# Optimization experiments

Hardware: AMD Instinct MI355X
Metric: run time of the kernel (lower is better)

## Reference

```python
import jax, jax.numpy as jnp
from jax import lax
import numpy as np

B, HW = 256, 64          # batch, image side (grayscale)
L, E, K = 32, 64, 8192   # latent_size, embedding_size, num_embeddings
DN = ('NHWC', 'HWIO', 'NHWC')


def setup_inputs() -> dict:
    key = jax.random.key(0)
    ks = jax.random.split(key, 21)
    n = lambda k, shape, s=0.05: (jax.random.normal(k, shape, jnp.float32) * s)
    return {
        'x': jax.random.uniform(ks[0], (B, HW, HW), jnp.float32),
        # encoder convs (SAME, stride 2): 64->32->16->8
        'enc_w1': n(ks[1], (4, 4, 1, 32)),   'enc_b1': jnp.zeros((32,), jnp.float32),
        'enc_w2': n(ks[2], (4, 4, 32, 64)),  'enc_b2': jnp.zeros((64,), jnp.float32),
        'enc_w3': n(ks[3], (4, 4, 64, 128)), 'enc_b3': jnp.zeros((128,), jnp.float32),
        # encoder dense: flatten 8*8*128=8192 -> 512 -> L*E=2048
        'fc_w': n(ks[4], (8192, 512), 0.02), 'fc_b': jnp.zeros((512,), jnp.float32),
        'ffc_w': n(ks[5], (512, L * E), 0.02), 'ffc_b': jnp.zeros((L * E,), jnp.float32),
        # VQ codebook
        'embeds': n(ks[6], (K, E), 0.02),
        # decoder dense: 2048 -> 512, then 1x1x512 feature map
        'dec_fc_w': n(ks[7], (L * E, 512), 0.02), 'dec_fc_b': jnp.zeros((512,), jnp.float32),
        # decoder conv_transpose VALID: 1->4->16->64
        'dec_w1': n(ks[8], (4, 4, 512, 256)),  'dec_b1': jnp.zeros((256,), jnp.float32),
        'dec_w2': n(ks[9], (4, 4, 256, 128)),  'dec_b2': jnp.zeros((128,), jnp.float32),
        'dec_w3': n(ks[10], (4, 4, 128, 1)),   'dec_b3': jnp.zeros((1,), jnp.float32),
    }


def _conv(h, w, b, s):
    return jax.nn.relu(lax.conv_general_dilated(h, w, (s, s), 'SAME', dimension_numbers=DN) + b)


def reference(x, enc_w1, enc_b1, enc_w2, enc_b2, enc_w3, enc_b3,
              fc_w, fc_b, ffc_w, ffc_b, embeds,
              dec_fc_w, dec_fc_b, dec_w1, dec_b1, dec_w2, dec_b2, dec_w3, dec_b3):
    # ---- encoder ----
    h = x[..., None]                                   # (B,64,64,1)
    h = _conv(h, enc_w1, enc_b1, 2)                    # (B,32,32,32)
    h = _conv(h, enc_w2, enc_b2, 2)                    # (B,16,16,64)
    h = _conv(h, enc_w3, enc_b3, 2)                    # (B,8,8,128)
    h = h.reshape(h.shape[0], -1)                      # (B,8192)
    h = jax.nn.relu(h @ fc_w + fc_b)                   # (B,512)
    pred = jax.nn.relu(h @ ffc_w + ffc_b).reshape(-1, L, E)  # (B,L,E)
    # ---- VQ middle: nearest codebook entry (argmin of L2 norm == argmin of squared dist) ----
    d2 = (jnp.sum(pred * pred, axis=-1, keepdims=True)
          - 2.0 * jnp.einsum('ble,ke->blk', pred, embeds)
          + jnp.sum(embeds * embeds, axis=-1))         # (B,L,K)
    classes = jnp.argmin(d2, axis=-1)                  # (B,L) int
    collected = embeds[classes]                        # (B,L,E) gather
    h = collected.reshape(-1, L * E)                   # (B,2048)
    # ---- decoder ----
    h = jax.nn.relu(h @ dec_fc_w + dec_fc_b)           # (B,512)
    h = h[:, None, None, :]                            # (B,1,1,512)
    h = jax.nn.relu(lax.conv_transpose(h, dec_w1, (1, 1), 'VALID', dimension_numbers=DN) + dec_b1)  # (B,4,4,256)
    h = jax.nn.relu(lax.conv_transpose(h, dec_w2, (4, 4), 'VALID', dimension_numbers=DN) + dec_b2)  # (B,16,16,128)
    out = lax.conv_transpose(h, dec_w3, (4, 4), 'VALID', dimension_numbers=DN) + dec_b3             # (B,64,64,1)
    return out  # L2 loss_type: output_t = logits_t
```

## Files before the change

kernel.cpp:

```cpp
#include <hip/hip_runtime.h>
#include <cfloat>


typedef short bf16x8 __attribute__((ext_vector_type(8)));
typedef float f32x4 __attribute__((ext_vector_type(4)));
#define MFMA16(a, b, c) __builtin_amdgcn_mfma_f32_16x16x32_bf16(a, b, c, 0, 0, 0)

__device__ inline unsigned short f2bf(float x) {
  unsigned u = __float_as_uint(x);
  u += 0x7fffu + ((u >> 16) & 1u);
  return (unsigned short)(u >> 16);
}
__device__ inline float bf2f(unsigned short h) {
  return __uint_as_float(((unsigned)h) << 16);
}
__device__ inline void split3v(float v, unsigned short& hb, unsigned short& mb,
                               unsigned short& lb) {
  hb = f2bf(v);
  float r1 = v - bf2f(hb);
  mb = f2bf(r1);
  lb = f2bf(r1 - bf2f(mb));
}

__global__ __launch_bounds__(256) void k_zborder(unsigned short* __restrict__ base,
                                                 int W, size_t planeElems,
                                                 int logC) {
  int bc = blockIdx.x * 256 + threadIdx.x;
  int C = 1 << logC;
  int b = bc >> logC, c = bc & (C - 1);
  int i = blockIdx.y, row, col;
  if (i < W) { row = 0; col = i; }
  else if (i < 2 * W) { row = W - 1; col = i - W; }
  else { int j = i - 2 * W; row = 1 + (j >> 1); col = (j & 1) ? W - 1 : 0; }
  base[blockIdx.z * planeElems + ((size_t)(b * W + row) * W + col) * C + c] = 0;
}

__global__ __launch_bounds__(256) void k_conv1(const float* __restrict__ x,
                                               const float* __restrict__ w,
                                               const float* __restrict__ bias,
                                               unsigned short* __restrict__ oH,
                                               unsigned short* __restrict__ oM,
                                               unsigned short* __restrict__ oL) {
  int b = blockIdx.x >> 5;
  int y = blockIdx.x & 31;
  int t = threadIdx.x;
  int c = t & 31;
  int xg = t >> 5;
  float acc[4] = {0.f, 0.f, 0.f, 0.f};
  for (int dy = 0; dy < 4; ++dy) {
    int iy = 2 * y + dy - 1;
    if (iy < 0 || iy >= 64) continue;
    const float* xrow = x + ((size_t)b * 64 + iy) * 64;
    for (int dx = 0; dx < 4; ++dx) {
      float wv = w[(dy * 4 + dx) * 32 + c];
#pragma unroll
      for (int i = 0; i < 4; ++i) {
        int ix = 8 * xg + 2 * i + dx - 1;
        float v = (ix >= 0 && ix < 64) ? xrow[ix] : 0.f;
        acc[i] = fmaf(v, wv, acc[i]);
      }
    }
  }
  float bv = bias[c];
#pragma unroll
  for (int i = 0; i < 4; ++i) {
    float v = acc[i] + bv;
    v = v > 0.f ? v : 0.f;
    unsigned short hb, mb, lb;
    split3v(v, hb, mb, lb);
    size_t o = ((size_t)(b * 34 + y + 1) * 34 + (4 * xg + i + 1)) * 32 + c;
    oH[o] = hb; oM[o] = mb; oL[o] = lb;
  }
}

__global__ __launch_bounds__(256) void k_wprep2(const float* __restrict__ w,
                                                unsigned short* __restrict__ H,
                                                unsigned short* __restrict__ M,
                                                unsigned short* __restrict__ L) {
  int idx = blockIdx.x * 256 + threadIdx.x;
  int j = idx & 7, lane = (idx >> 3) & 63, nt = (idx >> 9) & 3, s = idx >> 11;
  int ci = ((lane >> 4) << 3) + j, co = (nt << 4) + (lane & 15);
  unsigned short hb, mb, lb;
  split3v(w[(s * 32 + ci) * 64 + co], hb, mb, lb);
  H[idx] = hb; M[idx] = mb; L[idx] = lb;
}
__global__ __launch_bounds__(256) void k_wprep3(const float* __restrict__ w,
                                                unsigned short* __restrict__ H,
                                                unsigned short* __restrict__ M,
                                                unsigned short* __restrict__ L) {
  int idx = blockIdx.x * 256 + threadIdx.x;
  int j = idx & 7, lane = (idx >> 3) & 63, ks = (idx >> 9) & 1;
  int nt = (idx >> 10) & 3, ch = (idx >> 12) & 1, s = idx >> 13;
  int ci = ks * 32 + ((lane >> 4) << 3) + j;
  int co = ch * 64 + (nt << 4) + (lane & 15);
  unsigned short hb, mb, lb;
  split3v(w[(s * 64 + ci) * 128 + co], hb, mb, lb);
  H[idx] = hb; M[idx] = mb; L[idx] = lb;
}

__global__ __launch_bounds__(256) void k_conv2m(
    const unsigned short* __restrict__ aH, const unsigned short* __restrict__ aM,
    const unsigned short* __restrict__ aL, const unsigned short* __restrict__ wH,
    const unsigned short* __restrict__ wM, const unsigned short* __restrict__ wL,
    const float* __restrict__ bias, unsigned short* __restrict__ oH,
    unsigned short* __restrict__ oM, unsigned short* __restrict__ oL) {
  int t = threadIdx.x;
  int wave = t >> 6, lane = t & 63;
  int l15 = lane & 15, quad = lane >> 4;
  int m0 = blockIdx.x * 64 + wave * 16;
  int p = m0 + l15;
  int b = p >> 8, y = (p >> 4) & 15, x = p & 15;
  f32x4 acc[4] = {};
  for (int s = 0; s < 16; ++s) {
    int dy = s >> 2, dx = s & 3;
    size_t aoff = ((size_t)(b * 34 + 2 * y + dy) * 34 + (2 * x + dx)) * 32 + quad * 8;
    bf16x8 ah = *(const bf16x8*)(aH + aoff);
    bf16x8 am = *(const bf16x8*)(aM + aoff);
    bf16x8 al = *(const bf16x8*)(aL + aoff);
#pragma unroll
    for (int nt = 0; nt < 4; ++nt) {
      size_t woff = ((size_t)(s * 4 + nt) * 64 + lane) * 8;
      bf16x8 bh = *(const bf16x8*)(wH + woff);
      bf16x8 bm = *(const bf16x8*)(wM + woff);
      bf16x8 bl = *(const bf16x8*)(wL + woff);
      acc[nt] = MFMA16(am, bm, acc[nt]);
      acc[nt] = MFMA16(ah, bl, acc[nt]);
      acc[nt] = MFMA16(al, bh, acc[nt]);
      acc[nt] = MFMA16(ah, bm, acc[nt]);
      acc[nt] = MFMA16(am, bh, acc[nt]);
      acc[nt] = MFMA16(ah, bh, acc[nt]);
    }
  }
#pragma unroll
  for (int r = 0; r < 4; ++r) {
    int pp = m0 + quad * 4 + r;
    int b2 = pp >> 8, yo = (pp >> 4) & 15, xo = pp & 15;
    size_t obase = ((size_t)(b2 * 18 + yo + 1) * 18 + (xo + 1)) * 64;
#pragma unroll
    for (int nt = 0; nt < 4; ++nt) {
      int co = nt * 16 + l15;
      float v = acc[nt][r] + bias[co];
      v = v > 0.f ? v : 0.f;
      unsigned short hb, mb, lb;
      split3v(v, hb, mb, lb);
      oH[obase + co] = hb; oM[obase + co] = mb; oL[obase + co] = lb;
    }
  }
}

__global__ __launch_bounds__(256) void k_conv3m(
    const unsigned short* __restrict__ aH, const unsigned short* __restrict__ aM,
    const unsigned short* __restrict__ aL, const unsigned short* __restrict__ wH,
    const unsigned short* __restrict__ wM, const unsigned short* __restrict__ wL,
    const float* __restrict__ bias, unsigned short* __restrict__ oH,
    unsigned short* __restrict__ oM, unsigned short* __restrict__ oL) {
  int t = threadIdx.x;
  int wave = t >> 6, lane = t & 63;
  int l15 = lane & 15, quad = lane >> 4;
  int pg = wave >> 1, ch = wave & 1;
  int m0 = blockIdx.x * 64 + pg * 32;
  f32x4 acc[2][4] = {};
  for (int s = 0; s < 16; ++s) {
    int dy = s >> 2, dx = s & 3;
    bf16x8 ah[2][2], am[2][2], al[2][2];
#pragma unroll
    for (int mt = 0; mt < 2; ++mt) {
      int p = m0 + mt * 16 + l15;
      int b = p >> 6, y = (p >> 3) & 7, x = p & 7;
      size_t base = ((size_t)(b * 18 + 2 * y + dy) * 18 + (2 * x + dx)) * 64 + quad * 8;
#pragma unroll
      for (int ks = 0; ks < 2; ++ks) {
        ah[mt][ks] = *(const bf16x8*)(aH + base + ks * 32);
        am[mt][ks] = *(const bf16x8*)(aM + base + ks * 32);
        al[mt][ks] = *(const bf16x8*)(aL + base + ks * 32);
      }
    }
#pragma unroll
    for (int nt = 0; nt < 4; ++nt) {
#pragma unroll
      for (int ks = 0; ks < 2; ++ks) {
        size_t woff = ((size_t)((((s * 2 + ch) * 4 + nt) * 2 + ks) * 64 + lane)) * 8;
        bf16x8 bh = *(const bf16x8*)(wH + woff);
        bf16x8 bm = *(const bf16x8*)(wM + woff);
        bf16x8 bl = *(const bf16x8*)(wL + woff);
#pragma unroll
        for (int mt = 0; mt < 2; ++mt) {
          acc[mt][nt] = MFMA16(am[mt][ks], bm, acc[mt][nt]);
          acc[mt][nt] = MFMA16(ah[mt][ks], bl, acc[mt][nt]);
          acc[mt][nt] = MFMA16(al[mt][ks], bh, acc[mt][nt]);
          acc[mt][nt] = MFMA16(ah[mt][ks], bm, acc[mt][nt]);
          acc[mt][nt] = MFMA16(am[mt][ks], bh, acc[mt][nt]);
          acc[mt][nt] = MFMA16(ah[mt][ks], bh, acc[mt][nt]);
        }
      }
    }
  }
#pragma unroll
  for (int mt = 0; mt < 2; ++mt)
#pragma unroll
    for (int nt = 0; nt < 4; ++nt) {
      int co = ch * 64 + nt * 16 + l15;
      float bv = bias[co];
#pragma unroll
      for (int r = 0; r < 4; ++r) {
        int pp = m0 + mt * 16 + quad * 4 + r;
        float v = acc[mt][nt][r] + bv;
        v = v > 0.f ? v : 0.f;
        unsigned short hb, mb, lb;
        split3v(v, hb, mb, lb);
        size_t o = (size_t)pp * 128 + co;
        oH[o] = hb; oM[o] = mb; oL[o] = lb;
      }
    }
}

__global__ __launch_bounds__(256) void k_bprep(const float* __restrict__ w,
                                               unsigned short* __restrict__ Bp,
                                               int K, int N, int NP) {
  int idx = blockIdx.x * 256 + threadIdx.x;
  if (idx >= NP * K * N) return;
  int j = idx & 7, lane = (idx >> 3) & 63;
  int f = idx >> 9;
  int NT = N >> 4, KT = K >> 5;
  int ntg = f % NT; f /= NT;
  int kt = f % KT; int s = f / KT;
  int k = kt * 32 + ((lane >> 4) << 3) + j;
  int n = ntg * 16 + (lane & 15);
  unsigned short hb, mb, lb;
  split3v(w[(size_t)k * N + n], hb, mb, lb);
  Bp[idx] = s == 0 ? hb : (s == 1 ? mb : lb);
}

__global__ __launch_bounds__(256) void k_bprep_ct(const float* __restrict__ w,
                                                  unsigned short* __restrict__ Bp,
                                                  int K, int N, int oshift,
                                                  int NP) {
  int idx = blockIdx.x * 256 + threadIdx.x;
  if (idx >= NP * K * N) return;
  int j = idx & 7, lane = (idx >> 3) & 63;
  int f = idx >> 9;
  int NT = N >> 4, KT = K >> 5;
  int ntg = f % NT; f /= NT;
  int kt = f % KT; int s = f / KT;
  int k = kt * 32 + ((lane >> 4) << 3) + j;
  int n = ntg * 16 + (lane & 15);
  int o = n & ((1 << oshift) - 1), ru = n >> oshift;
  int r = ru >> 2, u = ru & 3;
  int sf = (3 - r) * 4 + (3 - u);
  unsigned short hb, mb, lb;
  split3v(w[(((size_t)sf * K + k) << oshift) + o], hb, mb, lb);
  Bp[idx] = s == 0 ? hb : (s == 1 ? mb : lb);
}

template <int NP, int NTW>
__global__ __launch_bounds__(256) void k_mgemm(
    const unsigned short* __restrict__ A0, const unsigned short* __restrict__ A1,
    const unsigned short* __restrict__ A2, const unsigned short* __restrict__ Bp,
    float* __restrict__ C, const float* __restrict__ bias,
    int M, int N, int K, int bmask) {
  int S = gridDim.z;
  int Kc = K / S;
  int t = threadIdx.x;
  int wave = t >> 6, lane = t & 63;
  int l15 = lane & 15, quad = lane >> 4;
  int m0 = blockIdx.x * 64 + wave * 16;
  int n0 = blockIdx.y * (16 * NTW);
  int KT = K >> 5, NT = N >> 4;
  int kt0 = (blockIdx.z * Kc) >> 5;
  int ktn = Kc >> 5;
  size_t sstride = (size_t)KT * NT * 512;
  const unsigned short* arow0 = A0 + (size_t)(m0 + l15) * K + quad * 8;
  const unsigned short* arow1 = A1 + (size_t)(m0 + l15) * K + quad * 8;
  const unsigned short* arow2 = nullptr;
  if constexpr (NP == 3) arow2 = A2 + (size_t)(m0 + l15) * K + quad * 8;
  f32x4 acc[NTW] = {};
  for (int kt = kt0; kt < kt0 + ktn; ++kt) {
    bf16x8 ah = *(const bf16x8*)(arow0 + kt * 32);
    bf16x8 am = *(const bf16x8*)(arow1 + kt * 32);
    bf16x8 al;
    if constexpr (NP == 3) al = *(const bf16x8*)(arow2 + kt * 32);
    const unsigned short* bbase =
        Bp + ((size_t)kt * NT + (n0 >> 4)) * 512 + lane * 8;
#pragma unroll
    for (int nt = 0; nt < NTW; ++nt) {
      const unsigned short* bp = bbase + nt * 512;
      bf16x8 bh = *(const bf16x8*)(bp);
      bf16x8 bm = *(const bf16x8*)(bp + sstride);
      if constexpr (NP == 3) {
        bf16x8 bl = *(const bf16x8*)(bp + 2 * sstride);
        acc[nt] = MFMA16(am, bm, acc[nt]);
        acc[nt] = MFMA16(ah, bl, acc[nt]);
        acc[nt] = MFMA16(al, bh, acc[nt]);
        acc[nt] = MFMA16(ah, bm, acc[nt]);
        acc[nt] = MFMA16(am, bh, acc[nt]);
        acc[nt] = MFMA16(ah, bh, acc[nt]);
      } else {
        acc[nt] = MFMA16(ah, bm, acc[nt]);
        acc[nt] = MFMA16(am, bh, acc[nt]);
        acc[nt] = MFMA16(ah, bh, acc[nt]);
      }
    }
  }
  if (S == 1) {
#pragma unroll
    for (int nt = 0; nt < NTW; ++nt) {
      int n = n0 + nt * 16 + l15;
      float bv = bias[n & bmask];
#pragma unroll
      for (int r = 0; r < 4; ++r) {
        int m = m0 + quad * 4 + r;
        float v = acc[nt][r] + bv;
        C[(size_t)m * N + n] = v > 0.f ? v : 0.f;
      }
    }
  } else {
    float* Cp = C + (size_t)blockIdx.z * M * N;
#pragma unroll
    for (int nt = 0; nt < NTW; ++nt) {
      int n = n0 + nt * 16 + l15;
#pragma unroll
      for (int r = 0; r < 4; ++r) {
        int m = m0 + quad * 4 + r;
        Cp[(size_t)m * N + n] = acc[nt][r];
      }
    }
  }
}

template <int NPOUT>
__global__ __launch_bounds__(256) void k_sumrelu3(
    const float* __restrict__ part, const float* __restrict__ bias,
    unsigned short* __restrict__ oH, unsigned short* __restrict__ oM,
    unsigned short* __restrict__ oL, int MN, int bmask, int S) {
  int idx = blockIdx.x * 256 + threadIdx.x;
  float s = 0.f;
  for (int z = 0; z < S; ++z) s += part[(size_t)z * MN + idx];
  s += bias[idx & bmask];
  s = s > 0.f ? s : 0.f;
  unsigned short hb = f2bf(s);
  float r1 = s - bf2f(hb);
  unsigned short mb = f2bf(r1);
  oH[idx] = hb; oM[idx] = mb;
  if constexpr (NPOUT == 3) oL[idx] = f2bf(r1 - bf2f(mb));
}

__global__ __launch_bounds__(256) void k_norm2(const float* __restrict__ e,
                                               float* __restrict__ n2) {
  int k = blockIdx.x * 256 + threadIdx.x;
  const float4* p = (const float4*)(e + (size_t)k * 64);
  float s0 = 0, s1 = 0, s2 = 0, s3 = 0;
#pragma unroll
  for (int j = 0; j < 16; ++j) {
    float4 v = p[j];
    s0 = fmaf(v.x, v.x, s0); s1 = fmaf(v.y, v.y, s1);
    s2 = fmaf(v.z, v.z, s2); s3 = fmaf(v.w, v.w, s3);
  }
  n2[k] = (s0 + s1) + (s2 + s3);
}

__global__ __launch_bounds__(256) void k_eprep(const float* __restrict__ e,
                                               unsigned short* __restrict__ Bp) {
  int idx = blockIdx.x * 256 + threadIdx.x;
  int j = idx & 7, lane = (idx >> 3) & 63;
  int f = idx >> 9;
  int s = f % 3; f /= 3;
  int nt = f % 4; f /= 4;
  int ks = f % 2; int kt = f / 2;
  int code = kt * 64 + nt * 16 + (lane & 15);
  int k = ks * 32 + ((lane >> 4) << 3) + j;
  unsigned short hb, mb, lb;
  split3v(e[(size_t)code * 64 + k], hb, mb, lb);
  Bp[idx] = s == 0 ? hb : (s == 1 ? mb : lb);
}

__global__ __launch_bounds__(256) void k_vqmfma3(
    const unsigned short* __restrict__ pH, const unsigned short* __restrict__ pM,
    const unsigned short* __restrict__ pL, const unsigned short* __restrict__ eB,
    const float* __restrict__ n2, float* __restrict__ pbd, int* __restrict__ pbk) {
  int t = threadIdx.x;
  int wave = t >> 6, lane = t & 63;
  int l15 = lane & 15, quad = lane >> 4;
  int m0 = blockIdx.x * 128 + wave * 32;
  int z = blockIdx.y;
  bf16x8 ah[2][2], am[2][2], al[2][2];
#pragma unroll
  for (int mt = 0; mt < 2; ++mt) {
    size_t arow = (size_t)(m0 + mt * 16 + l15) * 64 + quad * 8;
#pragma unroll
    for (int ks = 0; ks < 2; ++ks) {
      ah[mt][ks] = *(const bf16x8*)(pH + arow + ks * 32);
      am[mt][ks] = *(const bf16x8*)(pM + arow + ks * 32);
      al[mt][ks] = *(const bf16x8*)(pL + arow + ks * 32);
    }
  }
  float bd[2][4]; int bk[2][4];
#pragma unroll
  for (int mt = 0; mt < 2; ++mt)
#pragma unroll
    for (int r = 0; r < 4; ++r) { bd[mt][r] = FLT_MAX; bk[mt][r] = 0; }
  for (int kt = z * 16; kt < z * 16 + 16; ++kt) {
    const unsigned short* bb = eB + (size_t)kt * 12288 + lane * 8;
    f32x4 acc[2][4] = {};
#pragma unroll
    for (int ks = 0; ks < 2; ++ks)
#pragma unroll
      for (int nt = 0; nt < 4; ++nt) {
        const unsigned short* bp = bb + ((ks * 4 + nt) * 3) * 512;
        bf16x8 bh = *(const bf16x8*)(bp);
        bf16x8 bm = *(const bf16x8*)(bp + 512);
        bf16x8 bl = *(const bf16x8*)(bp + 1024);
#pragma unroll
        for (int mt = 0; mt < 2; ++mt) {
          acc[mt][nt] = MFMA16(am[mt][ks], bm, acc[mt][nt]);
          acc[mt][nt] = MFMA16(ah[mt][ks], bl, acc[mt][nt]);
          acc[mt][nt] = MFMA16(al[mt][ks], bh, acc[mt][nt]);
          acc[mt][nt] = MFMA16(ah[mt][ks], bm, acc[mt][nt]);
          acc[mt][nt] = MFMA16(am[mt][ks], bh, acc[mt][nt]);
          acc[mt][nt] = MFMA16(ah[mt][ks], bh, acc[mt][nt]);
        }
      }
    int cb = kt * 64;
#pragma unroll
    for (int nt = 0; nt < 4; ++nt) {
      int code = cb + nt * 16 + l15;
      float nv = n2[code];
#pragma unroll
      for (int mt = 0; mt < 2; ++mt)
#pragma unroll
        for (int r = 0; r < 4; ++r) {
          float d = fmaf(-2.f, acc[mt][nt][r], nv);
          if (d < bd[mt][r]) { bd[mt][r] = d; bk[mt][r] = code; }
        }
    }
  }
#pragma unroll
  for (int mt = 0; mt < 2; ++mt)
#pragma unroll
    for (int r = 0; r < 4; ++r)
#pragma unroll
      for (int s = 1; s < 16; s <<= 1) {
        float od = __shfl_xor(bd[mt][r], s);
        int ok = __shfl_xor(bk[mt][r], s);
        if (od < bd[mt][r] || (od == bd[mt][r] && ok < bk[mt][r])) {
          bd[mt][r] = od; bk[mt][r] = ok;
        }
      }
  if (l15 == 0) {
#pragma unroll
    for (int mt = 0; mt < 2; ++mt)
#pragma unroll
      for (int r = 0; r < 4; ++r) {
        pbd[(size_t)z * 8192 + m0 + mt * 16 + quad * 4 + r] = bd[mt][r];
        pbk[(size_t)z * 8192 + m0 + mt * 16 + quad * 4 + r] = bk[mt][r];
      }
  }
}

__global__ __launch_bounds__(256) void k_vqgather(const float* __restrict__ pbd,
                                                  const int* __restrict__ pbk,
                                                  const float* __restrict__ embeds,
                                                  unsigned short* __restrict__ cH,
                                                  unsigned short* __restrict__ cM) {
  int idx = blockIdx.x * 256 + threadIdx.x;
  int m = idx >> 6;
  float bd = pbd[m]; int bk = pbk[m];
#pragma unroll
  for (int z = 1; z < 8; ++z) {
    float d = pbd[(size_t)z * 8192 + m]; int k = pbk[(size_t)z * 8192 + m];
    if (d < bd || (d == bd && k < bk)) { bd = d; bk = k; }
  }
  float v = embeds[(size_t)bk * 64 + (idx & 63)];
  unsigned short hb = f2bf(v);
  cH[idx] = hb;
  cM[idx] = f2bf(v - bf2f(hb));
}

__global__ __launch_bounds__(256) void k_dec3(const float* __restrict__ d2buf,
                                              const float* __restrict__ w3,
                                              const float* __restrict__ b3,
                                              float* __restrict__ out) {
  __shared__ float sx[16 * 129];
  __shared__ float wT[128 * 16];
  int b = blockIdx.x >> 4;
  int y = blockIdx.x & 15;
  int t = threadIdx.x;
#pragma unroll
  for (int j = 0; j < 8; ++j) {
    int idx = t + j * 256;
    int xx = idx >> 7, c = idx & 127;
    size_t m2 = ((size_t)b * 4 + (y >> 2)) * 4 + (xx >> 2);
    sx[xx * 129 + c] = d2buf[m2 * 2048 + ((y & 3) * 4 + (xx & 3)) * 128 + c];
  }
#pragma unroll
  for (int j = 0; j < 8; ++j) {
    int idx = t + j * 256;
    int c = idx >> 4, ru = idx & 15;
    int R = ru >> 2, U = ru & 3;
    wT[c * 16 + ru] = w3[((3 - R) * 4 + (3 - U)) * 128 + c];
  }
  __syncthreads();
  int xx = t >> 4, ru = t & 15;
  float a0 = 0, a1 = 0, a2 = 0, a3 = 0;
#pragma unroll 8
  for (int c = 0; c < 128; c += 4) {
    a0 = fmaf(sx[xx * 129 + c + 0], wT[(c + 0) * 16 + ru], a0);
    a1 = fmaf(sx[xx * 129 + c + 1], wT[(c + 1) * 16 + ru], a1);
    a2 = fmaf(sx[xx * 129 + c + 2], wT[(c + 2) * 16 + ru], a2);
    a3 = fmaf(sx[xx * 129 + c + 3], wT[(c + 3) * 16 + ru], a3);
  }
  float acc = (a0 + a1) + (a2 + a3) + b3[0];
  int R = ru >> 2, U = ru & 3;
  out[((size_t)b * 64 + 4 * y + R) * 64 + 4 * xx + U] = acc;
}

extern "C" void kernel_launch(void* const* d_in, const int* in_sizes, int n_in,
                              void* d_out, int out_size, void* d_ws, size_t ws_size,
                              hipStream_t stream) {
  const float* x        = (const float*)d_in[0];
  const float* enc_w1   = (const float*)d_in[1];
  const float* enc_b1   = (const float*)d_in[2];
  const float* enc_w2   = (const float*)d_in[3];
  const float* enc_b2   = (const float*)d_in[4];
  const float* enc_w3   = (const float*)d_in[5];
  const float* enc_b3   = (const float*)d_in[6];
  const float* fc_w     = (const float*)d_in[7];
  const float* fc_b     = (const float*)d_in[8];
  const float* ffc_w    = (const float*)d_in[9];
  const float* ffc_b    = (const float*)d_in[10];
  const float* embeds   = (const float*)d_in[11];
  const float* dec_fc_w = (const float*)d_in[12];
  const float* dec_fc_b = (const float*)d_in[13];
  const float* dec_w1   = (const float*)d_in[14];
  const float* dec_b1   = (const float*)d_in[15];
  const float* dec_w2   = (const float*)d_in[16];
  const float* dec_b2   = (const float*)d_in[17];
  const float* dec_w3   = (const float*)d_in[18];
  const float* dec_b3   = (const float*)d_in[19];
  float* outp = (float*)d_out;

  char* ws = (char*)d_ws;
  size_t off = 0;
  auto alloc = [&](size_t bytes) { size_t r = off; off = (off + bytes + 255) & ~(size_t)255; return r; };

  size_t RA = alloc(57147392);
  unsigned short* h1pH = (unsigned short*)(ws + RA);
  unsigned short* h1pM = (unsigned short*)(ws + RA + 18939904);
  unsigned short* h1pL = (unsigned short*)(ws + RA + 37879808);
  float* d2buf            = (float*)(ws + RA);
  float* partials         = (float*)(ws + RA + 33554432);
  unsigned short* Bp_d1   = (unsigned short*)(ws + RA + 41943040);
  unsigned short* d1H     = (unsigned short*)(ws + RA + 50331648);
  unsigned short* d1M     = (unsigned short*)(ws + RA + 52428800);
  unsigned short* hdH     = (unsigned short*)(ws + RA + 54525952);
  unsigned short* hdM     = (unsigned short*)(ws + RA + 54788096);
  unsigned short* cH      = (unsigned short*)(ws + RA + 55050240);
  unsigned short* cM      = (unsigned short*)(ws + RA + 56098816);

  size_t RB = alloc(31850496);
  unsigned short* h2pH = (unsigned short*)(ws + RB);
  unsigned short* h2pM = (unsigned short*)(ws + RB + 10616832);
  unsigned short* h2pL = (unsigned short*)(ws + RB + 21233664);
  unsigned short* Bp_fc = (unsigned short*)(ws + RB);
  unsigned short* eB    = (unsigned short*)(ws + RB + 25165824);
  unsigned short* pH    = (unsigned short*)(ws + RB + 28311552);
  unsigned short* pM    = (unsigned short*)(ws + RB + 29360128);
  unsigned short* pL    = (unsigned short*)(ws + RB + 30408704);

  size_t RC = alloc(12582912);
  unsigned short* h3H = (unsigned short*)(ws + RC);
  unsigned short* h3M = (unsigned short*)(ws + RC + 4194304);
  unsigned short* h3L = (unsigned short*)(ws + RC + 8388608);
  unsigned short* Bp_ffc = (unsigned short*)(ws + RC);
  unsigned short* hfcH   = (unsigned short*)(ws + RC + 6291456);
  unsigned short* hfcM   = (unsigned short*)(ws + RC + 6553600);
  unsigned short* hfcL   = (unsigned short*)(ws + RC + 6815744);
  unsigned short* Bp_dfc = (unsigned short*)(ws + RC);
  unsigned short* Bp_d2  = (unsigned short*)(ws + RC + 4194304);

  float* n2buf   = (float*)(ws + alloc(32768));
  float* pbd     = (float*)(ws + alloc(262144));
  int*   pbk     = (int*)  (ws + alloc(262144));
  unsigned short* Wp2H = (unsigned short*)(ws + alloc(196608));
  unsigned short* Wp2M = Wp2H + 32768;
  unsigned short* Wp2L = Wp2M + 32768;
  unsigned short* Wp3H = (unsigned short*)(ws + alloc(786432));
  unsigned short* Wp3M = Wp3H + 131072;
  unsigned short* Wp3L = Wp3M + 131072;
  (void)ws_size; (void)in_sizes; (void)n_in; (void)out_size;

  k_zborder<<<dim3(32, 132, 3), 256, 0, stream>>>(h1pH, 34, 9469952, 5);
  k_zborder<<<dim3(64, 68, 3), 256, 0, stream>>>(h2pH, 18, 5308416, 6);

  k_wprep2<<<128, 256, 0, stream>>>(enc_w2, Wp2H, Wp2M, Wp2L);
  k_wprep3<<<512, 256, 0, stream>>>(enc_w3, Wp3H, Wp3M, Wp3L);

  k_conv1<<<8192, 256, 0, stream>>>(x, enc_w1, enc_b1, h1pH, h1pM, h1pL);
  k_conv2m<<<1024, 256, 0, stream>>>(h1pH, h1pM, h1pL, Wp2H, Wp2M, Wp2L,
                                     enc_b2, h2pH, h2pM, h2pL);
  k_conv3m<<<256, 256, 0, stream>>>(h2pH, h2pM, h2pL, Wp3H, Wp3M, Wp3L,
                                    enc_b3, h3H, h3M, h3L);

  k_bprep<<<49152, 256, 0, stream>>>(fc_w, Bp_fc, 8192, 512, 3);
  k_eprep<<<6144, 256, 0, stream>>>(embeds, eB);
  k_norm2<<<32, 256, 0, stream>>>(embeds, n2buf);
  k_mgemm<3, 4><<<dim3(4, 8, 16), 256, 0, stream>>>(
      h3H, h3M, h3L, Bp_fc, partials, fc_b, 256, 512, 8192, 511);
  k_bprep<<<12288, 256, 0, stream>>>(ffc_w, Bp_ffc, 512, 2048, 3);
  k_sumrelu3<3><<<512, 256, 0, stream>>>(partials, fc_b, hfcH, hfcM, hfcL,
                                         131072, 511, 16);
  k_mgemm<3, 4><<<dim3(4, 32, 4), 256, 0, stream>>>(
      hfcH, hfcM, hfcL, Bp_ffc, partials, ffc_b, 256, 2048, 512, 2047);
  k_bprep<<<8192, 256, 0, stream>>>(dec_fc_w, Bp_dfc, 2048, 512, 2);
  k_sumrelu3<3><<<2048, 256, 0, stream>>>(partials, ffc_b, pH, pM, pL,
                                          524288, 2047, 4);

  k_vqmfma3<<<dim3(64, 8), 256, 0, stream>>>(pH, pM, pL, eB, n2buf, pbd, pbk);
  k_vqgather<<<2048, 256, 0, stream>>>(pbd, pbk, embeds, cH, cM);

  k_mgemm<2, 4><<<dim3(4, 8, 16), 256, 0, stream>>>(
      cH, cM, nullptr, Bp_dfc, partials, dec_fc_b, 256, 512, 2048, 511);
  k_sumrelu3<2><<<512, 256, 0, stream>>>(partials, dec_fc_b, hdH, hdM, nullptr,
                                         131072, 511, 16);

  k_bprep_ct<<<16384, 256, 0, stream>>>(dec_w1, Bp_d1, 512, 4096, 8, 2);
  k_mgemm<2, 4><<<dim3(4, 64, 2), 256, 0, stream>>>(
      hdH, hdM, nullptr, Bp_d1, partials, dec_b1, 256, 4096, 512, 255);
  k_sumrelu3<2><<<4096, 256, 0, stream>>>(partials, dec_b1, d1H, d1M, nullptr,
                                          1048576, 255, 2);

  k_bprep_ct<<<4096, 256, 0, stream>>>(dec_w2, Bp_d2, 256, 2048, 7, 2);
  k_mgemm<2, 8><<<dim3(64, 16, 1), 256, 0, stream>>>(
      d1H, d1M, nullptr, Bp_d2, d2buf, dec_b2, 4096, 2048, 256, 127);

  k_dec3<<<4096, 256, 0, stream>>>(d2buf, dec_w3, dec_b3, outp);
}
```

Measured before the change: 526.1 us.

## Merge prep kernels, split conv3 over K, and use shift-based index math

Fuses the border zeroing, conv weight prep, codebook prep, norm computation and two decoder weight preps into one early launch, which cuts kernel launch count and lets small kernels share the GPU. Conv3 is split across two K-halves with more blocks (512x2) writing fp32 partials, followed by a sum-relu-split pass, to raise parallelism. The bprep kernels replace div/mod with shifts and masks. Buffers are reallocated so the early-prepped weights are not overwritten. This adds an extra partials round trip for conv3.

```diff
diff --git a/kernel.cpp b/kernel.cpp
--- a/kernel.cpp
+++ b/kernel.cpp
@@ -22,17 +22,113 @@
   lb = f2bf(r1 - bf2f(mb));
 }
 
-__global__ __launch_bounds__(256) void k_zborder(unsigned short* __restrict__ base,
-                                                 int W, size_t planeElems,
-                                                 int logC) {
-  int bc = blockIdx.x * 256 + threadIdx.x;
-  int C = 1 << logC;
-  int b = bc >> logC, c = bc & (C - 1);
-  int i = blockIdx.y, row, col;
-  if (i < W) { row = 0; col = i; }
-  else if (i < 2 * W) { row = W - 1; col = i - W; }
-  else { int j = i - 2 * W; row = 1 + (j >> 1); col = (j & 1) ? W - 1 : 0; }
-  base[blockIdx.z * planeElems + ((size_t)(b * W + row) * W + col) * C + c] = 0;
+#define PB0 12672
+#define PB1 (PB0 + 13056)
+#define PB2 (PB1 + 128)
+#define PB3 (PB2 + 512)
+#define PB4 (PB3 + 6144)
+#define PB5 (PB4 + 32)
+#define PB6 (PB5 + 8192)
+#define PB7 (PB6 + 4096)
+__global__ __launch_bounds__(256) void k_prep_early(
+    const float* __restrict__ enc_w2, const float* __restrict__ enc_w3,
+    const float* __restrict__ embeds, const float* __restrict__ dec_fc_w,
+    const float* __restrict__ dec_w2, unsigned short* __restrict__ h1base,
+    unsigned short* __restrict__ h2base, unsigned short* __restrict__ Wp2H,
+    unsigned short* __restrict__ Wp2M, unsigned short* __restrict__ Wp2L,
+    unsigned short* __restrict__ Wp3H, unsigned short* __restrict__ Wp3M,
+    unsigned short* __restrict__ Wp3L, unsigned short* __restrict__ eB,
+    float* __restrict__ n2, unsigned short* __restrict__ Bp_dfc,
+    unsigned short* __restrict__ Bp_d2) {
+  int blk = blockIdx.x;
+  int t = threadIdx.x;
+  if (blk < PB0) {
+    int li = blk * 256 + t;
+    int bc = li & 8191;
+    int rest = li >> 13;
+    int i = rest % 132, plane = rest / 132;
+    int b = bc >> 5, c = bc & 31;
+    int row, col;
+    if (i < 34) { row = 0; col = i; }
+    else if (i < 68) { row = 33; col = i - 34; }
+    else { int j = i - 68; row = 1 + (j >> 1); col = (j & 1) ? 33 : 0; }
+    h1base[(size_t)plane * 9469952 + ((size_t)(b * 34 + row) * 34 + col) * 32 + c] = 0;
+  } else if (blk < PB1) {
+    int li = (blk - PB0) * 256 + t;
+    int bc = li & 16383;
+    int rest = li >> 14;
+    int i = rest % 68, plane = rest / 68;
+    int b = bc >> 6, c = bc & 63;
+    int row, col;
+    if (i < 18) { row = 0; col = i; }
+    else if (i < 36) { row = 17; col = i - 18; }
+    else { int j = i - 36; row = 1 + (j >> 1); col = (j & 1) ? 17 : 0; }
+    h2base[(size_t)plane * 5308416 + ((size_t)(b * 18 + row) * 18 + col) * 64 + c] = 0;
+  } else if (blk < PB2) {
+    int idx = (blk - PB1) * 256 + t;
+    int j = idx & 7, lane = (idx >> 3) & 63, nt = (idx >> 9) & 3, s = idx >> 11;
+    int ci = ((lane >> 4) << 3) + j, co = (nt << 4) + (lane & 15);
+    unsigned short hb, mb, lb;
+    split3v(enc_w2[(s * 32 + ci) * 64 + co], hb, mb, lb);
+    Wp2H[idx] = hb; Wp2M[idx] = mb; Wp2L[idx] = lb;
+  } else if (blk < PB3) {
+    int idx = (blk - PB2) * 256 + t;
+    int j = idx & 7, lane = (idx >> 3) & 63, ks = (idx >> 9) & 1;
+    int nt = (idx >> 10) & 3, ch = (idx >> 12) & 1, s = idx >> 13;
+    int ci = ks * 32 + ((lane >> 4) << 3) + j;
+    int co = ch * 64 + (nt << 4) + (lane & 15);
+    unsigned short hb, mb, lb;
+    split3v(enc_w3[(s * 64 + ci) * 128 + co], hb, mb, lb);
+    Wp3H[idx] = hb; Wp3M[idx] = mb; Wp3L[idx] = lb;
+  } else if (blk < PB4) {
+    int idx = (blk - PB3) * 256 + t;
+    int j = idx & 7, lane = (idx >> 3) & 63;
+    int f = idx >> 9;
+    int s = f % 3; f /= 3;
+    int nt = f & 3; f >>= 2;
+    int ks = f & 1; int kt = f >> 1;
+    int code = kt * 64 + nt * 16 + (lane & 15);
+    int k = ks * 32 + ((lane >> 4) << 3) + j;
+    unsigned short hb, mb, lb;
+    split3v(embeds[(size_t)code * 64 + k], hb, mb, lb);
+    eB[idx] = s == 0 ? hb : (s == 1 ? mb : lb);
+  } else if (blk < PB5) {
+    int k = (blk - PB4) * 256 + t;
+    const float4* p = (const float4*)(embeds + (size_t)k * 64);
+    float s0 = 0, s1 = 0, s2 = 0, s3 = 0;
+#pragma unroll
+    for (int j = 0; j < 16; ++j) {
+      float4 v = p[j];
+      s0 = fmaf(v.x, v.x, s0); s1 = fmaf(v.y, v.y, s1);
+      s2 = fmaf(v.z, v.z, s2); s3 = fmaf(v.w, v.w, s3);
+    }
+    n2[k] = (s0 + s1) + (s2 + s3);
+  } else if (blk < PB6) {
+    int idx = (blk - PB5) * 256 + t;
+    int j = idx & 7, lane = (idx >> 3) & 63;
+    int f = idx >> 9;
+    int ntg = f & 31; f >>= 5;
+    int kt = f & 63; int s = f >> 6;
+    int k = kt * 32 + ((lane >> 4) << 3) + j;
+    int n = ntg * 16 + (lane & 15);
+    unsigned short hb, mb, lb;
+    split3v(dec_fc_w[(size_t)k * 512 + n], hb, mb, lb);
+    Bp_dfc[idx] = s == 0 ? hb : mb;
+  } else if (blk < PB7) {
+    int idx = (blk - PB6) * 256 + t;
+    int j = idx & 7, lane = (idx >> 3) & 63;
+    int f = idx >> 9;
+    int ntg = f & 127; f >>= 7;
+    int kt = f & 7; int s = f >> 3;
+    int k = kt * 32 + ((lane >> 4) << 3) + j;
+    int n = ntg * 16 + (lane & 15);
+    int o = n & 127, ru = n >> 7;
+    int r = ru >> 2, u = ru & 3;
+    int sf = (3 - r) * 4 + (3 - u);
+    unsigned short hb, mb, lb;
+    split3v(dec_w2[(((size_t)sf * 256 + k) << 7) + o], hb, mb, lb);
+    Bp_d2[idx] = s == 0 ? hb : mb;
+  }
 }
 
 __global__ __launch_bounds__(256) void k_conv1(const float* __restrict__ x,
@@ -71,31 +167,6 @@
     size_t o = ((size_t)(b * 34 + y + 1) * 34 + (4 * xg + i + 1)) * 32 + c;
     oH[o] = hb; oM[o] = mb; oL[o] = lb;
   }
-}
-
-__global__ __launch_bounds__(256) void k_wprep2(const float* __restrict__ w,
-                                                unsigned short* __restrict__ H,
-                                                unsigned short* __restrict__ M,
-                                                unsigned short* __restrict__ L) {
-  int idx = blockIdx.x * 256 + threadIdx.x;
-  int j = idx & 7, lane = (idx >> 3) & 63, nt = (idx >> 9) & 3, s = idx >> 11;
-  int ci = ((lane >> 4) << 3) + j, co = (nt << 4) + (lane & 15);
-  unsigned short hb, mb, lb;
-  split3v(w[(s * 32 + ci) * 64 + co], hb, mb, lb);
-  H[idx] = hb; M[idx] = mb; L[idx] = lb;
-}
-__global__ __launch_bounds__(256) void k_wprep3(const float* __restrict__ w,
-                                                unsigned short* __restrict__ H,
-                                                unsigned short* __restrict__ M,
-                                                unsigned short* __restrict__ L) {
-  int idx = blockIdx.x * 256 + threadIdx.x;
-  int j = idx & 7, lane = (idx >> 3) & 63, ks = (idx >> 9) & 1;
-  int nt = (idx >> 10) & 3, ch = (idx >> 12) & 1, s = idx >> 13;
-  int ci = ks * 32 + ((lane >> 4) << 3) + j;
-  int co = ch * 64 + (nt << 4) + (lane & 15);
-  unsigned short hb, mb, lb;
-  split3v(w[(s * 64 + ci) * 128 + co], hb, mb, lb);
-  H[idx] = hb; M[idx] = mb; L[idx] = lb;
 }
 
 __global__ __launch_bounds__(256) void k_conv2m(
@@ -152,28 +223,25 @@
     const unsigned short* __restrict__ aH, const unsigned short* __restrict__ aM,
     const unsigned short* __restrict__ aL, const unsigned short* __restrict__ wH,
     const unsigned short* __restrict__ wM, const unsigned short* __restrict__ wL,
-    const float* __restrict__ bias, unsigned short* __restrict__ oH,
-    unsigned short* __restrict__ oM, unsigned short* __restrict__ oL) {
+    float* __restrict__ part) {
   int t = threadIdx.x;
   int wave = t >> 6, lane = t & 63;
   int l15 = lane & 15, quad = lane >> 4;
-  int pg = wave >> 1, ch = wave & 1;
-  int m0 = blockIdx.x * 64 + pg * 32;
-  f32x4 acc[2][4] = {};
-  for (int s = 0; s < 16; ++s) {
+  int mtg = wave & 1, ch = wave >> 1;
+  int m0 = blockIdx.x * 32 + mtg * 16;
+  int z = blockIdx.y;
+  int p = m0 + l15;
+  int b = p >> 6, y = (p >> 3) & 7, x = p & 7;
+  f32x4 acc[4] = {};
+  for (int s = z * 8; s < z * 8 + 8; ++s) {
     int dy = s >> 2, dx = s & 3;
-    bf16x8 ah[2][2], am[2][2], al[2][2];
-#pragma unroll
-    for (int mt = 0; mt < 2; ++mt) {
-      int p = m0 + mt * 16 + l15;
-      int b = p >> 6, y = (p >> 3) & 7, x = p & 7;
-      size_t base = ((size_t)(b * 18 + 2 * y + dy) * 18 + (2 * x + dx)) * 64 + quad * 8;
-#pragma unroll
-      for (int ks = 0; ks < 2; ++ks) {
-        ah[mt][ks] = *(const bf16x8*)(aH + base + ks * 32);
-        am[mt][ks] = *(const bf16x8*)(aM + base + ks * 32);
-        al[mt][ks] = *(const bf16x8*)(aL + base + ks * 32);
-      }
+    size_t base = ((size_t)(b * 18 + 2 * y + dy) * 18 + (2 * x + dx)) * 64 + quad * 8;
+    bf16x8 ah[2], am[2], al[2];
+#pragma unroll
+    for (int ks = 0; ks < 2; ++ks) {
+      ah[ks] = *(const bf16x8*)(aH + base + ks * 32);
+      am[ks] = *(const bf16x8*)(aM + base + ks * 32);
+      al[ks] = *(const bf16x8*)(aL + base + ks * 32);
     }
 #pragma unroll
     for (int nt = 0; nt < 4; ++nt) {
@@ -183,47 +251,35 @@
         bf16x8 bh = *(const bf16x8*)(wH + woff);
         bf16x8 bm = *(const bf16x8*)(wM + woff);
         bf16x8 bl = *(const bf16x8*)(wL + woff);
-#pragma unroll
-        for (int mt = 0; mt < 2; ++mt) {
-          acc[mt][nt] = MFMA16(am[mt][ks], bm, acc[mt][nt]);
-          acc[mt][nt] = MFMA16(ah[mt][ks], bl, acc[mt][nt]);
-          acc[mt][nt] = MFMA16(al[mt][ks], bh, acc[mt][nt]);
-          acc[mt][nt] = MFMA16(ah[mt][ks], bm, acc[mt][nt]);
-          acc[mt][nt] = MFMA16(am[mt][ks], bh, acc[mt][nt]);
-          acc[mt][nt] = MFMA16(ah[mt][ks], bh, acc[mt][nt]);
-        }
-      }
-    }
-  }
-#pragma unroll
-  for (int mt = 0; mt < 2; ++mt)
-#pragma unroll
-    for (int nt = 0; nt < 4; ++nt) {
-      int co = ch * 64 + nt * 16 + l15;
-      float bv = bias[co];
-#pragma unroll
-      for (int r = 0; r < 4; ++r) {
-        int pp = m0 + mt * 16 + quad * 4 + r;
-        float v = acc[mt][nt][r] + bv;
-        v = v > 0.f ? v : 0.f;
-        unsigned short hb, mb, lb;
-        split3v(v, hb, mb, lb);
-        size_t o = (size_t)pp * 128 + co;
-        oH[o] = hb; oM[o] = mb; oL[o] = lb;
-      }
-    }
+        acc[nt] = MFMA16(am[ks], bm, acc[nt]);
+        acc[nt] = MFMA16(ah[ks], bl, acc[nt]);
+        acc[nt] = MFMA16(al[ks], bh, acc[nt]);
+        acc[nt] = MFMA16(ah[ks], bm, acc[nt]);
+        acc[nt] = MFMA16(am[ks], bh, acc[nt]);
+        acc[nt] = MFMA16(ah[ks], bh, acc[nt]);
+      }
+    }
+  }
+  float* Cp = part + (size_t)z * 2097152;
+#pragma unroll
+  for (int nt = 0; nt < 4; ++nt) {
+    int co = ch * 64 + nt * 16 + l15;
+#pragma unroll
+    for (int r = 0; r < 4; ++r) {
+      int pp = m0 + quad * 4 + r;
+      Cp[(size_t)pp * 128 + co] = acc[nt][r];
+    }
+  }
 }
 
 __global__ __launch_bounds__(256) void k_bprep(const float* __restrict__ w,
                                                unsigned short* __restrict__ Bp,
-                                               int K, int N, int NP) {
+                                               int logNT, int logKT, int N) {
   int idx = blockIdx.x * 256 + threadIdx.x;
-  if (idx >= NP * K * N) return;
   int j = idx & 7, lane = (idx >> 3) & 63;
   int f = idx >> 9;
-  int NT = N >> 4, KT = K >> 5;
-  int ntg = f % NT; f /= NT;
-  int kt = f % KT; int s = f / KT;
+  int ntg = f & ((1 << logNT) - 1); f >>= logNT;
+  int kt = f & ((1 << logKT) - 1); int s = f >> logKT;
   int k = kt * 32 + ((lane >> 4) << 3) + j;
   int n = ntg * 16 + (lane & 15);
   unsigned short hb, mb, lb;
@@ -233,15 +289,13 @@
 
 __global__ __launch_bounds__(256) void k_bprep_ct(const float* __restrict__ w,
                                                   unsigned short* __restrict__ Bp,
-                                                  int K, int N, int oshift,
-                                                  int NP) {
+                                                  int logNT, int logKT, int K,
+                                                  int oshift) {
   int idx = blockIdx.x * 256 + threadIdx.x;
-  if (idx >= NP * K * N) return;
   int j = idx & 7, lane = (idx >> 3) & 63;
   int f = idx >> 9;
-  int NT = N >> 4, KT = K >> 5;
-  int ntg = f % NT; f /= NT;
-  int kt = f % KT; int s = f / KT;
+  int ntg = f & ((1 << logNT) - 1); f >>= logNT;
+  int kt = f & ((1 << logKT) - 1); int s = f >> logKT;
   int k = kt * 32 + ((lane >> 4) << 3) + j;
   int n = ntg * 16 + (lane & 15);
   int o = n & ((1 << oshift) - 1), ru = n >> oshift;
@@ -344,35 +398,6 @@
   if constexpr (NPOUT == 3) oL[idx] = f2bf(r1 - bf2f(mb));
 }
 
-__global__ __launch_bounds__(256) void k_norm2(const float* __restrict__ e,
-                                               float* __restrict__ n2) {
-  int k = blockIdx.x * 256 + threadIdx.x;
-  const float4* p = (const float4*)(e + (size_t)k * 64);
-  float s0 = 0, s1 = 0, s2 = 0, s3 = 0;
-#pragma unroll
-  for (int j = 0; j < 16; ++j) {
-    float4 v = p[j];
-    s0 = fmaf(v.x, v.x, s0); s1 = fmaf(v.y, v.y, s1);
-    s2 = fmaf(v.z, v.z, s2); s3 = fmaf(v.w, v.w, s3);
-  }
-  n2[k] = (s0 + s1) + (s2 + s3);
-}
-
-__global__ __launch_bounds__(256) void k_eprep(const float* __restrict__ e,
-                                               unsigned short* __restrict__ Bp) {
-  int idx = blockIdx.x * 256 + threadIdx.x;
-  int j = idx & 7, lane = (idx >> 3) & 63;
-  int f = idx >> 9;
-  int s = f % 3; f /= 3;
-  int nt = f % 4; f /= 4;
-  int ks = f % 2; int kt = f / 2;
-  int code = kt * 64 + nt * 16 + (lane & 15);
-  int k = ks * 32 + ((lane >> 4) << 3) + j;
-  unsigned short hb, mb, lb;
-  split3v(e[(size_t)code * 64 + k], hb, mb, lb);
-  Bp[idx] = s == 0 ? hb : (s == 1 ? mb : lb);
-}
-
 __global__ __launch_bounds__(256) void k_vqmfma3(
     const unsigned short* __restrict__ pH, const unsigned short* __restrict__ pM,
     const unsigned short* __restrict__ pL, const unsigned short* __restrict__ eB,
@@ -548,7 +573,7 @@
   unsigned short* h1pL = (unsigned short*)(ws + RA + 37879808);
   float* d2buf            = (float*)(ws + RA);
   float* partials         = (float*)(ws + RA + 33554432);
-  unsigned short* Bp_d1   = (unsigned short*)(ws + RA + 41943040);
+  unsigned short* Bp_d1   = (unsigned short*)(ws + RA + 50331648 - 8388608);
   unsigned short* d1H     = (unsigned short*)(ws + RA + 50331648);
   unsigned short* d1M     = (unsigned short*)(ws + RA + 52428800);
   unsigned short* hdH     = (unsigned short*)(ws + RA + 54525952);
@@ -561,7 +586,6 @@
   unsigned short* h2pM = (unsigned short*)(ws + RB + 10616832);
   unsigned short* h2pL = (unsigned short*)(ws + RB + 21233664);
   unsigned short* Bp_fc = (unsigned short*)(ws + RB);
-  unsigned short* eB    = (unsigned short*)(ws + RB + 25165824);
   unsigned short* pH    = (unsigned short*)(ws + RB + 28311552);
   unsigned short* pM    = (unsigned short*)(ws + RB + 29360128);
   unsigned short* pL    = (unsigned short*)(ws + RB + 30408704);
@@ -574,9 +598,10 @@
   unsigned short* hfcH   = (unsigned short*)(ws + RC + 6291456);
   unsigned short* hfcM   = (unsigned short*)(ws + RC + 6553600);
   unsigned short* hfcL   = (unsigned short*)(ws + RC + 6815744);
-  unsigned short* Bp_dfc = (unsigned short*)(ws + RC);
-  unsigned short* Bp_d2  = (unsigned short*)(ws + RC + 4194304);
-
+
+  unsigned short* eB     = (unsigned short*)(ws + alloc(3145728));
+  unsigned short* Bp_dfc = (unsigned short*)(ws + alloc(4194304));
+  unsigned short* Bp_d2  = (unsigned short*)(ws + alloc(2097152));
   float* n2buf   = (float*)(ws + alloc(32768));
   float* pbd     = (float*)(ws + alloc(262144));
   int*   pbk     = (int*)  (ws + alloc(262144));
@@ -588,29 +613,26 @@
   unsigned short* Wp3L = Wp3M + 131072;
   (void)ws_size; (void)in_sizes; (void)n_in; (void)out_size;
 
-  k_zborder<<<dim3(32, 132, 3), 256, 0, stream>>>(h1pH, 34, 9469952, 5);
-  k_zborder<<<dim3(64, 68, 3), 256, 0, stream>>>(h2pH, 18, 5308416, 6);
-
-  k_wprep2<<<128, 256, 0, stream>>>(enc_w2, Wp2H, Wp2M, Wp2L);
-  k_wprep3<<<512, 256, 0, stream>>>(enc_w3, Wp3H, Wp3M, Wp3L);
+  k_prep_early<<<PB7, 256, 0, stream>>>(
+      enc_w2, enc_w3, embeds, dec_fc_w, dec_w2, h1pH, h2pH,
+      Wp2H, Wp2M, Wp2L, Wp3H, Wp3M, Wp3L, eB, n2buf, Bp_dfc, Bp_d2);
 
   k_conv1<<<8192, 256, 0, stream>>>(x, enc_w1, enc_b1, h1pH, h1pM, h1pL);
   k_conv2m<<<1024, 256, 0, stream>>>(h1pH, h1pM, h1pL, Wp2H, Wp2M, Wp2L,
                                      enc_b2, h2pH, h2pM, h2pL);
-  k_conv3m<<<256, 256, 0, stream>>>(h2pH, h2pM, h2pL, Wp3H, Wp3M, Wp3L,
-                                    enc_b3, h3H, h3M, h3L);
-
-  k_bprep<<<49152, 256, 0, stream>>>(fc_w, Bp_fc, 8192, 512, 3);
-  k_eprep<<<6144, 256, 0, stream>>>(embeds, eB);
-  k_norm2<<<32, 256, 0, stream>>>(embeds, n2buf);
+  k_conv3m<<<dim3(512, 2), 256, 0, stream>>>(h2pH, h2pM, h2pL,
+                                             Wp3H, Wp3M, Wp3L, partials);
+  k_sumrelu3<3><<<8192, 256, 0, stream>>>(partials, enc_b3, h3H, h3M, h3L,
+                                          2097152, 127, 2);
+
+  k_bprep<<<49152, 256, 0, stream>>>(fc_w, Bp_fc, 5, 8, 512);
   k_mgemm<3, 4><<<dim3(4, 8, 16), 256, 0, stream>>>(
       h3H, h3M, h3L, Bp_fc, partials, fc_b, 256, 512, 8192, 511);
-  k_bprep<<<12288, 256, 0, stream>>>(ffc_w, Bp_ffc, 512, 2048, 3);
+  k_bprep<<<12288, 256, 0, stream>>>(ffc_w, Bp_ffc, 7, 4, 2048);
   k_sumrelu3<3><<<512, 256, 0, stream>>>(partials, fc_b, hfcH, hfcM, hfcL,
                                          131072, 511, 16);
   k_mgemm<3, 4><<<dim3(4, 32, 4), 256, 0, stream>>>(
       hfcH, hfcM, hfcL, Bp_ffc, partials, ffc_b, 256, 2048, 512, 2047);
-  k_bprep<<<8192, 256, 0, stream>>>(dec_fc_w, Bp_dfc, 2048, 512, 2);
   k_sumrelu3<3><<<2048, 256, 0, stream>>>(partials, ffc_b, pH, pM, pL,
                                           524288, 2047, 4);
 
@@ -622,13 +644,12 @@
   k_sumrelu3<2><<<512, 256, 0, stream>>>(partials, dec_fc_b, hdH, hdM, nullptr,
                                          131072, 511, 16);
 
-  k_bprep_ct<<<16384, 256, 0, stream>>>(dec_w1, Bp_d1, 512, 4096, 8, 2);
+  k_bprep_ct<<<16384, 256, 0, stream>>>(dec_w1, Bp_d1, 8, 4, 512, 8);
   k_mgemm<2, 4><<<dim3(4, 64, 2), 256, 0, stream>>>(
       hdH, hdM, nullptr, Bp_d1, partials, dec_b1, 256, 4096, 512, 255);
   k_sumrelu3<2><<<4096, 256, 0, stream>>>(partials, dec_b1, d1H, d1M, nullptr,
                                           1048576, 255, 2);
 
-  k_bprep_ct<<<4096, 256, 0, stream>>>(dec_w2, Bp_d2, 256, 2048, 7, 2);
   k_mgemm<2, 8><<<dim3(64, 16, 1), 256, 0, stream>>>(
       d1H, d1M, nullptr, Bp_d2, d2buf, dec_b2, 4096, 2048, 256, 127);
 
```

Measured after the change: 488.3 us. -7.2%, faster.
